# Kernel tuning notes

Measured on AMD Instinct MI355X. Metric: run time of the kernel, lower is better.

Reference implementation:

```python
import jax, jax.numpy as jnp
import numpy as np

B, D, C, OUT = 16384, 784, 2048, 10

def setup_inputs() -> dict:
    key = jax.random.key(0)
    k1, k2, k3 = jax.random.split(key, 3)
    x = jax.random.normal(k1, (B, D), dtype=jnp.float32)
    centres = jax.random.normal(k2, (C, D), dtype=jnp.float32)
    log_sigmas = jnp.zeros((C,), dtype=jnp.float32)
    W = jax.random.normal(k3, (OUT, C), dtype=jnp.float32) * (1.0 / np.sqrt(C))
    b = jnp.zeros((OUT,), dtype=jnp.float32)
    return {"x": x, "centres": centres, "log_sigmas": log_sigmas, "W": W, "b": b}

def reference(x, centres, log_sigmas, W, b):
    # (B, C, D) broadcast tensor the torch code materializes; same math).
    x2 = jnp.sum(x * x, axis=-1, keepdims=True)          # (B, 1)
    c2 = jnp.sum(centres * centres, axis=-1)             # (C,)
    d2 = jnp.maximum(x2 + c2[None, :] - 2.0 * (x @ centres.T), 0.0)  # (B, C)
    distances = jnp.sqrt(d2) / jnp.exp(log_sigmas)[None, :]          # (B, C)
    phi = jnp.exp(-(distances * distances))              # gaussian basis
    return phi @ W.T + b                                  # (B, OUT)
```

## Files before the change

### kernel.cpp

```cpp
#include <hip/hip_runtime.h>


#define B_ROWS 16384
#define D_DIM  784
#define C_DIM  2048
#define NOUT   10
#define KPAD   832
#define BK     64
#define NT     13

typedef __attribute__((ext_vector_type(8))) __bf16 bf16x8;
typedef __attribute__((ext_vector_type(4))) float  f32x4;
typedef __attribute__((ext_vector_type(4))) unsigned short ushort4v;

__device__ __forceinline__ unsigned short f2bf(float f) {
  union { float f; unsigned int u; } v; v.f = f;
  unsigned int u = v.u;
  return (unsigned short)((u + 0x7fffu + ((u >> 16) & 1u)) >> 16);
}

__device__ __forceinline__ void async16(const unsigned short* g, unsigned short* l) {
  __builtin_amdgcn_global_load_lds((const __attribute__((address_space(1))) void*)g,
                                   (__attribute__((address_space(3))) void*)l,
                                   16, 0, 0);
}

__device__ __forceinline__ void conv_row(const float* __restrict__ src,
                                         unsigned short* __restrict__ dst,
                                         float* __restrict__ sq, int row, int lane) {
  const float* s = src + (size_t)row * D_DIM;
  unsigned short* d = dst + (size_t)row * KPAD;
  float acc = 0.f;
#pragma unroll
  for (int c = 0; c < 4; ++c) {
    const int ch = lane + c * 64;
    if (ch < 196) {
      const float4 v = ((const float4*)s)[ch];
      ushort4v o; o.x = f2bf(v.x); o.y = f2bf(v.y); o.z = f2bf(v.z); o.w = f2bf(v.w);
      *(ushort4v*)(d + ch * 4) = o;
      acc += v.x * v.x + v.y * v.y + v.z * v.z + v.w * v.w;
    } else if (ch < 208) {
      ushort4v z = {0, 0, 0, 0};
      *(ushort4v*)(d + ch * 4) = z;
    }
  }
#pragma unroll
  for (int off = 32; off > 0; off >>= 1) acc += __shfl_down(acc, off);
  if (lane == 0) sq[row] = acc;
}

__global__ __launch_bounds__(256) void prep_all(
    const float* __restrict__ x, const float* __restrict__ cen,
    const float* __restrict__ ls, const float* __restrict__ W,
    const float* __restrict__ bias,
    unsigned short* __restrict__ xb, unsigned short* __restrict__ cb,
    unsigned short* __restrict__ wb,
    float* __restrict__ x2, float* __restrict__ c2, float* __restrict__ sc,
    float* __restrict__ out) {
  const int bx = blockIdx.x;
  if (bx < B_ROWS / 4) {
    conv_row(x, xb, x2, bx * 4 + (threadIdx.x >> 6), threadIdx.x & 63);
  } else if (bx < B_ROWS / 4 + C_DIM / 4) {
    conv_row(cen, cb, c2, (bx - B_ROWS / 4) * 4 + (threadIdx.x >> 6), threadIdx.x & 63);
  } else {
    const int i = (bx - (B_ROWS / 4 + C_DIM / 4)) * 256 + threadIdx.x;
    if (i < B_ROWS * NOUT) out[i] = bias[i % NOUT];
    const int j = i - B_ROWS * NOUT;
    if (j >= 0 && j < 16 * C_DIM)
      wb[j] = ((j >> 11) < NOUT) ? f2bf(W[(j >> 11) * C_DIM + (j & 2047)]) : (unsigned short)0;
    const int k = j - 16 * C_DIM;
    if (k >= 0 && k < C_DIM) sc[k] = __expf(-2.f * ls[k]);
  }
}

__global__ __launch_bounds__(512, 2) void rbf_main(
    const unsigned short* __restrict__ xb, const unsigned short* __restrict__ cb,
    const unsigned short* __restrict__ wb,
    const float* __restrict__ x2, const float* __restrict__ c2,
    const float* __restrict__ scale, float* __restrict__ out) {
  __shared__ __align__(16) char smem[138240];
  unsigned short* Ph = (unsigned short*)smem;
  float* x2s = (float*)(smem + 135168);
  float* c2s = (float*)(smem + 136192);
  float* scs = (float*)(smem + 137216);

  const int tid  = threadIdx.x;
  const int w    = tid >> 6;
  const int lane = tid & 63;
  const int q    = lane >> 4;
  const int l16  = lane & 15;
  const int swz  = l16 & 7;
  const int brow = blockIdx.x * 256;
  const int bcol = blockIdx.y * 256;
  const int wr   = (w >> 2) * 128;
  const int wc   = (w & 3) * 64;

  if (tid < 256) { c2s[tid] = c2[bcol + tid]; scs[tid] = scale[bcol + tid]; }
  else           { x2s[tid - 256] = x2[brow + tid - 256]; }

  const int srow = tid >> 3;
  const int skc  = (tid & 7) ^ (srow & 7);
  const unsigned short* gA = xb + (size_t)(brow + srow) * KPAD + skc * 8;
  const unsigned short* gB = cb + (size_t)(bcol + srow) * KPAD + skc * 8;
  const int ldst = w * 512;

#define STG_A(P, K0, R) async16(gA + (size_t)(R) * 64 * KPAD + (K0), (P) + (R) * 4096 + ldst)
#define STG_B(P, K0, R) async16(gB + (size_t)(R) * 64 * KPAD + (K0), (P) + (R) * 4096 + ldst)

  {
    unsigned short* A0 = (unsigned short*)smem;
    unsigned short* B0 = (unsigned short*)(smem + 32768);
    STG_B(B0, 0, 0); STG_B(B0, 0, 1); STG_B(B0, 0, 2); STG_B(B0, 0, 3);
    STG_A(A0, 0, 0); STG_A(A0, 0, 2); STG_A(A0, 0, 1); STG_A(A0, 0, 3);
  }
  asm volatile("s_waitcnt vmcnt(2) lgkmcnt(0)" ::: "memory");
  __builtin_amdgcn_s_barrier();

  f32x4 acc[8][4] = {};

#define LD_A(IH, KS)                                                        \
  _Pragma("unroll")                                                         \
  for (int ii = 0; ii < 4; ++ii)                                            \
    af[ii] = *(const bf16x8*)&As[(wr + (IH) * 64 + ii * 16 + l16) * 64 +    \
                                 ((((KS) * 4 + q) ^ swz) << 3)];
#define LD_B(KS)                                                            \
  _Pragma("unroll")                                                         \
  for (int j = 0; j < 4; ++j)                                               \
    bfr[j] = *(const bf16x8*)&Bs[(wc + j * 16 + l16) * 64 +                 \
                                 ((((KS) * 4 + q) ^ swz) << 3)];
#define MFMA16(IOFF)                                                        \
  __builtin_amdgcn_s_setprio(1);                                            \
  _Pragma("unroll")                                                         \
  for (int ii = 0; ii < 4; ++ii)                                            \
    _Pragma("unroll")                                                       \
    for (int j = 0; j < 4; ++j)                                             \
      acc[(IOFF) + ii][j] = __builtin_amdgcn_mfma_f32_16x16x32_bf16(        \
          af[ii], bfr[j], acc[(IOFF) + ii][j], 0, 0, 0);                    \
  __builtin_amdgcn_s_setprio(0);

  for (int t = 0; t < NT; ++t) {
    char* base_r = smem + (t & 1) * 65536;
    char* base_s = smem + ((t + 1) & 1) * 65536;
    unsigned short* As  = (unsigned short*)base_r;
    unsigned short* Bs  = (unsigned short*)(base_r + 32768);
    unsigned short* Asn = (unsigned short*)base_s;
    unsigned short* Bsn = (unsigned short*)(base_s + 32768);
    const int kn = (t + 1) * BK;
    const bool st = (t < NT - 1);
    bf16x8 af[4], bfr[4];

    LD_A(0, 0)
    LD_B(0)
    if (st) { STG_B(Bsn, kn, 0); STG_B(Bsn, kn, 1); }
    __builtin_amdgcn_s_barrier();
    MFMA16(0)
    if (st) asm volatile("s_waitcnt vmcnt(2)" ::: "memory");
    else    asm volatile("s_waitcnt vmcnt(0)" ::: "memory");
    __builtin_amdgcn_s_barrier();

    LD_A(1, 0)
    if (st) { STG_B(Bsn, kn, 2); STG_B(Bsn, kn, 3); }
    __builtin_amdgcn_s_barrier();
    MFMA16(4)
    __builtin_amdgcn_s_barrier();

    LD_A(0, 1)
    LD_B(1)
    if (st) { STG_A(Asn, kn, 0); STG_A(Asn, kn, 2); }
    __builtin_amdgcn_s_barrier();
    MFMA16(0)
    __builtin_amdgcn_s_barrier();

    LD_A(1, 1)
    if (st) { STG_A(Asn, kn, 1); STG_A(Asn, kn, 3); }
    __builtin_amdgcn_s_barrier();
    MFMA16(4)
    if (st) asm volatile("s_waitcnt vmcnt(2)" ::: "memory");
    __builtin_amdgcn_s_barrier();
  }

  __syncthreads();

#pragma unroll
  for (int i = 0; i < 8; ++i) {
#pragma unroll
    for (int j = 0; j < 4; ++j) {
      const int cl = wc + j * 16 + l16;
      const float c2v = c2s[cl];
      const float sc = scs[cl];
#pragma unroll
      for (int r = 0; r < 4; ++r) {
        const int rl = wr + i * 16 + q * 4 + r;
        float d2 = fmaxf(x2s[rl] + c2v - 2.f * acc[i][j][r], 0.f);
        Ph[rl * 264 + cl] = f2bf(__expf(-d2 * sc));
      }
    }
  }
  __syncthreads();

  f32x4 oacc[2] = {};
#pragma unroll
  for (int kk = 0; kk < 8; ++kk) {
    const bf16x8 bw = *(const bf16x8*)&wb[(size_t)l16 * C_DIM + bcol + kk * 32 + q * 8];
#pragma unroll
    for (int mi = 0; mi < 2; ++mi) {
      const bf16x8 ap = *(const bf16x8*)&Ph[(w * 32 + mi * 16 + l16) * 264 + kk * 32 + q * 8];
      oacc[mi] = __builtin_amdgcn_mfma_f32_16x16x32_bf16(ap, bw, oacc[mi], 0, 0, 0);
    }
  }
  if (l16 < NOUT) {
#pragma unroll
    for (int mi = 0; mi < 2; ++mi)
#pragma unroll
      for (int r = 0; r < 4; ++r) {
        const int grow = brow + w * 32 + mi * 16 + q * 4 + r;
        atomicAdd(&out[grow * NOUT + l16], oacc[mi][r]);
      }
  }
#undef STG_A
#undef STG_B
#undef LD_A
#undef LD_B
#undef MFMA16
}

extern "C" void kernel_launch(void* const* d_in, const int* in_sizes, int n_in,
                              void* d_out, int out_size, void* d_ws, size_t ws_size,
                              hipStream_t stream) {
  const float* x    = (const float*)d_in[0];
  const float* cen  = (const float*)d_in[1];
  const float* ls   = (const float*)d_in[2];
  const float* W    = (const float*)d_in[3];
  const float* bias = (const float*)d_in[4];
  float* out = (float*)d_out;

  unsigned char* ws = (unsigned char*)d_ws;
  unsigned short* xb  = (unsigned short*)(ws);
  unsigned short* cbf = (unsigned short*)(ws + 27262976);
  unsigned short* wb  = (unsigned short*)(ws + 30670848);
  float* x2 = (float*)(ws + 30736384);
  float* c2 = (float*)(ws + 30801920);
  float* sc = (float*)(ws + 30810112);

  const int prep_blocks = B_ROWS / 4 + C_DIM / 4 +
                          (B_ROWS * NOUT + 16 * C_DIM + C_DIM + 255) / 256;
  prep_all<<<prep_blocks, 256, 0, stream>>>(x, cen, ls, W, bias, xb, cbf, wb, x2, c2, sc, out);
  rbf_main<<<dim3(B_ROWS / 256, C_DIM / 256), 512, 0, stream>>>(xb, cbf, wb, x2, c2, sc, out);
}
```

Measured before the change: 157.5 us.

## Replace double-buffered BK=64 pipeline with 4-stage BK=32 async prefetch ring

Restructures the GEMM main loop from a two-buffer, 64-wide K step with four barrier-separated sub-phases into a four-slot ring of 32-wide K tiles, keeping three tiles in flight via global_load_lds. Each iteration now waits on vmcnt, issues one barrier, prefetches tile t+3, loads all fragments and runs 32 MFMAs. The aim is to cut barrier count per K element and deepen latency hiding. In exchange, each 32-wide iteration carries a full barrier, and fragment loads are less interleaved with MFMAs, which may expose LDS latency.

```diff
diff --git a/kernel.cpp b/kernel.cpp
--- a/kernel.cpp
+++ b/kernel.cpp
@@ -6,8 +6,7 @@
 #define C_DIM  2048
 #define NOUT   10
 #define KPAD   832
-#define BK     64
-#define NT     13
+#define NT32   26
 
 typedef __attribute__((ext_vector_type(8))) __bf16 bf16x8;
 typedef __attribute__((ext_vector_type(4))) float  f32x4;
@@ -89,7 +88,6 @@
   const int lane = tid & 63;
   const int q    = lane >> 4;
   const int l16  = lane & 15;
-  const int swz  = l16 & 7;
   const int brow = blockIdx.x * 256;
   const int bcol = blockIdx.y * 256;
   const int wr   = (w >> 2) * 128;
@@ -97,87 +95,52 @@
 
   if (tid < 256) { c2s[tid] = c2[bcol + tid]; scs[tid] = scale[bcol + tid]; }
   else           { x2s[tid - 256] = x2[brow + tid - 256]; }
-
-  const int srow = tid >> 3;
-  const int skc  = (tid & 7) ^ (srow & 7);
-  const unsigned short* gA = xb + (size_t)(brow + srow) * KPAD + skc * 8;
-  const unsigned short* gB = cb + (size_t)(bcol + srow) * KPAD + skc * 8;
-  const int ldst = w * 512;
-
-#define STG_A(P, K0, R) async16(gA + (size_t)(R) * 64 * KPAD + (K0), (P) + (R) * 4096 + ldst)
-#define STG_B(P, K0, R) async16(gB + (size_t)(R) * 64 * KPAD + (K0), (P) + (R) * 4096 + ldst)
-
-  {
-    unsigned short* A0 = (unsigned short*)smem;
-    unsigned short* B0 = (unsigned short*)(smem + 32768);
-    STG_B(B0, 0, 0); STG_B(B0, 0, 1); STG_B(B0, 0, 2); STG_B(B0, 0, 3);
-    STG_A(A0, 0, 0); STG_A(A0, 0, 2); STG_A(A0, 0, 1); STG_A(A0, 0, 3);
-  }
-  asm volatile("s_waitcnt vmcnt(2) lgkmcnt(0)" ::: "memory");
-  __builtin_amdgcn_s_barrier();
+  asm volatile("s_waitcnt vmcnt(0)" ::: "memory");
+
+  const int srow = tid >> 2;
+  const int soct = (tid & 3) ^ (srow & 3);
+  const unsigned short* sA = xb + (size_t)(brow + srow) * KPAD + soct * 8;
+  const unsigned short* sB = cb + (size_t)(bcol + srow) * KPAD + soct * 8;
+  const int wslot = w * 512;
+
+#define STG(T) { unsigned short* bb = (unsigned short*)(smem + ((T) & 3) * 32768); \
+    const int k0_ = (T) * 32;                                                      \
+    async16(sA + k0_,              bb         + wslot);                            \
+    async16(sA + 128*KPAD + k0_,   bb + 4096  + wslot);                            \
+    async16(sB + k0_,              bb + 8192  + wslot);                            \
+    async16(sB + 128*KPAD + k0_,   bb + 12288 + wslot); }
+
+  STG(0); STG(1); STG(2);
 
   f32x4 acc[8][4] = {};
-
-#define LD_A(IH, KS)                                                        \
-  _Pragma("unroll")                                                         \
-  for (int ii = 0; ii < 4; ++ii)                                            \
-    af[ii] = *(const bf16x8*)&As[(wr + (IH) * 64 + ii * 16 + l16) * 64 +    \
-                                 ((((KS) * 4 + q) ^ swz) << 3)];
-#define LD_B(KS)                                                            \
-  _Pragma("unroll")                                                         \
-  for (int j = 0; j < 4; ++j)                                               \
-    bfr[j] = *(const bf16x8*)&Bs[(wc + j * 16 + l16) * 64 +                 \
-                                 ((((KS) * 4 + q) ^ swz) << 3)];
-#define MFMA16(IOFF)                                                        \
-  __builtin_amdgcn_s_setprio(1);                                            \
-  _Pragma("unroll")                                                         \
-  for (int ii = 0; ii < 4; ++ii)                                            \
-    _Pragma("unroll")                                                       \
-    for (int j = 0; j < 4; ++j)                                             \
-      acc[(IOFF) + ii][j] = __builtin_amdgcn_mfma_f32_16x16x32_bf16(        \
-          af[ii], bfr[j], acc[(IOFF) + ii][j], 0, 0, 0);                    \
-  __builtin_amdgcn_s_setprio(0);
-
-  for (int t = 0; t < NT; ++t) {
-    char* base_r = smem + (t & 1) * 65536;
-    char* base_s = smem + ((t + 1) & 1) * 65536;
-    unsigned short* As  = (unsigned short*)base_r;
-    unsigned short* Bs  = (unsigned short*)(base_r + 32768);
-    unsigned short* Asn = (unsigned short*)base_s;
-    unsigned short* Bsn = (unsigned short*)(base_s + 32768);
-    const int kn = (t + 1) * BK;
-    const bool st = (t < NT - 1);
-    bf16x8 af[4], bfr[4];
-
-    LD_A(0, 0)
-    LD_B(0)
-    if (st) { STG_B(Bsn, kn, 0); STG_B(Bsn, kn, 1); }
+  const int osw = (q ^ (l16 & 3)) << 3;
+
+  for (int t = 0; t < NT32; ++t) {
+    if (t < NT32 - 2)       asm volatile("s_waitcnt vmcnt(8)" ::: "memory");
+    else if (t == NT32 - 2) asm volatile("s_waitcnt vmcnt(4)" ::: "memory");
+    else                    asm volatile("s_waitcnt vmcnt(0)" ::: "memory");
     __builtin_amdgcn_s_barrier();
-    MFMA16(0)
-    if (st) asm volatile("s_waitcnt vmcnt(2)" ::: "memory");
-    else    asm volatile("s_waitcnt vmcnt(0)" ::: "memory");
-    __builtin_amdgcn_s_barrier();
-
-    LD_A(1, 0)
-    if (st) { STG_B(Bsn, kn, 2); STG_B(Bsn, kn, 3); }
-    __builtin_amdgcn_s_barrier();
-    MFMA16(4)
-    __builtin_amdgcn_s_barrier();
-
-    LD_A(0, 1)
-    LD_B(1)
-    if (st) { STG_A(Asn, kn, 0); STG_A(Asn, kn, 2); }
-    __builtin_amdgcn_s_barrier();
-    MFMA16(0)
-    __builtin_amdgcn_s_barrier();
-
-    LD_A(1, 1)
-    if (st) { STG_A(Asn, kn, 1); STG_A(Asn, kn, 3); }
-    __builtin_amdgcn_s_barrier();
-    MFMA16(4)
-    if (st) asm volatile("s_waitcnt vmcnt(2)" ::: "memory");
-    __builtin_amdgcn_s_barrier();
-  }
+
+    if (t < NT32 - 3) STG(t + 3);
+
+    const unsigned short* As = (const unsigned short*)(smem + (t & 3) * 32768);
+    const unsigned short* Bs = As + 8192;
+    bf16x8 af[8], bfr[4];
+#pragma unroll
+    for (int i = 0; i < 8; ++i)
+      af[i] = *(const bf16x8*)&As[(wr + i * 16 + l16) * 32 + osw];
+#pragma unroll
+    for (int j = 0; j < 4; ++j)
+      bfr[j] = *(const bf16x8*)&Bs[(wc + j * 16 + l16) * 32 + osw];
+    __builtin_amdgcn_s_setprio(1);
+#pragma unroll
+    for (int i = 0; i < 8; ++i)
+#pragma unroll
+      for (int j = 0; j < 4; ++j)
+        acc[i][j] = __builtin_amdgcn_mfma_f32_16x16x32_bf16(af[i], bfr[j], acc[i][j], 0, 0, 0);
+    __builtin_amdgcn_s_setprio(0);
+  }
+#undef STG
 
   __syncthreads();
 
@@ -217,11 +180,6 @@
         atomicAdd(&out[grow * NOUT + l16], oacc[mi][r]);
       }
   }
-#undef STG_A
-#undef STG_B
-#undef LD_A
-#undef LD_B
-#undef MFMA16
 }
 
 extern "C" void kernel_launch(void* const* d_in, const int* in_sizes, int n_in,
```

Result: slower. 167.0 us (+6.0%).
